# Kernel optimization log

Measured on AMD Instinct MI355X. Metric: run time of the kernel, lower is better.

## Reference

```python
import jax, jax.numpy as jnp
import numpy as np

B, H, S, D = 4, 16, 2048, 64

def setup_inputs() -> dict:
    key = jax.random.key(0)
    kq, kk, kv, km = jax.random.split(key, 4)
    q = jax.random.normal(kq, (B, H, S, D), dtype=jnp.float32)
    k = jax.random.normal(kk, (B, H, S, D), dtype=jnp.float32)
    v = jax.random.normal(kv, (B, H, S, D), dtype=jnp.float32)
    mask = jax.random.randint(km, (B, H, S, S), 0, 2, dtype=jnp.int32)
    return {"q": q, "k": k, "v": v, "mask": mask}

def reference(q, k, v, mask):
    d_k = q.shape[-1]
    scale = 1.0 / jnp.sqrt(jnp.asarray(d_k, dtype=q.dtype))
    # scores: [B, H, Sq, Sk]
    scores = jnp.einsum('bhqd,bhkd->bhqk', q, k) * scale
    scores = jnp.where(mask == 0, jnp.asarray(-10000.0, dtype=scores.dtype), scores)
    attn = jax.nn.softmax(scores, axis=-1)
    out = jnp.einsum('bhqk,bhkd->bhqd', attn, v)
    return (out, attn)
```

## Files before the change

kernel.cpp:

```cpp
#include <hip/hip_runtime.h>
#include <hip/hip_bf16.h>

typedef short bf16x8 __attribute__((ext_vector_type(8)));
typedef float f32x4 __attribute__((ext_vector_type(4)));
typedef unsigned short u16x8 __attribute__((ext_vector_type(8)));

#define DEVI static __device__ __forceinline__

constexpr int Bb = 4, Hh = 16, Ss = 2048, Dd = 64;
constexpr int BH = Bb * Hh;
constexpr float SCALE = 0.125f;
constexpr long QKV_ELEMS = (long)BH * Ss * Dd;
constexpr long MASK_ELEMS = (long)BH * Ss * Ss;

DEVI unsigned short f2bf(float f) {
  __hip_bfloat16 h = __float2bfloat16(f);
  unsigned short u;
  __builtin_memcpy(&u, &h, 2);
  return u;
}
DEVI float bflo(unsigned int u) { unsigned int x = u << 16;        float f; __builtin_memcpy(&f, &x, 4); return f; }
DEVI float bfhi(unsigned int u) { unsigned int x = u & 0xffff0000u; float f; __builtin_memcpy(&f, &x, 4); return f; }

DEVI int pidx(int q, int k) { return (q << 12) + ((k << 1) ^ ((q & 7) << 4)); }

DEVI bf16x8 cvt8(const float* p) {
  float4 a = *reinterpret_cast<const float4*>(p);
  float4 b = *reinterpret_cast<const float4*>(p + 4);
  bf16x8 r;
  r[0] = (short)f2bf(a.x); r[1] = (short)f2bf(a.y); r[2] = (short)f2bf(a.z); r[3] = (short)f2bf(a.w);
  r[4] = (short)f2bf(b.x); r[5] = (short)f2bf(b.y); r[6] = (short)f2bf(b.z); r[7] = (short)f2bf(b.w);
  return r;
}

__global__ __launch_bounds__(256) void bitpack(const int* __restrict__ mask,
                                               unsigned long long* __restrict__ bits)
{
  const long wid = (((long)blockIdx.x * 256 + threadIdx.x) >> 6);
  const int lane = threadIdx.x & 63;
  const long NW = ((long)gridDim.x * 256) >> 6;
  for (long W = wid; W < (MASK_ELEMS >> 8); W += NW) {
    const int* p = mask + (W << 8) + lane;
    const unsigned long long b0 = __ballot(__builtin_nontemporal_load(p) != 0);
    const unsigned long long b1 = __ballot(__builtin_nontemporal_load(p + 64) != 0);
    const unsigned long long b2 = __ballot(__builtin_nontemporal_load(p + 128) != 0);
    const unsigned long long b3 = __ballot(__builtin_nontemporal_load(p + 192) != 0);
    if (lane == 0) {
      ulonglong4 o; o.x = b0; o.y = b1; o.z = b2; o.w = b3;
      *reinterpret_cast<ulonglong4*>(bits + (W << 2)) = o;
    }
  }
}

__global__ __launch_bounds__(256) void cvt_qk(const float* __restrict__ q, const float* __restrict__ k,
                                              unsigned short* __restrict__ qb, unsigned short* __restrict__ kb)
{
  const long i = ((long)blockIdx.x * 256 + threadIdx.x) * 4;
  if (i >= QKV_ELEMS) return;
  const float4 a = *reinterpret_cast<const float4*>(q + i);
  ushort4 oa; oa.x = f2bf(a.x); oa.y = f2bf(a.y); oa.z = f2bf(a.z); oa.w = f2bf(a.w);
  *reinterpret_cast<ushort4*>(qb + i) = oa;
  const float4 b = *reinterpret_cast<const float4*>(k + i);
  ushort4 ob; ob.x = f2bf(b.x); ob.y = f2bf(b.y); ob.z = f2bf(b.z); ob.w = f2bf(b.w);
  *reinterpret_cast<ushort4*>(kb + i) = ob;
}

__global__ __launch_bounds__(256) void cvt_vt(const float* __restrict__ v, unsigned short* __restrict__ vt)
{
  __shared__ float tile[64][65];
  const int bh = blockIdx.x >> 5;
  const int s0 = (blockIdx.x & 31) << 6;
  const int t  = threadIdx.x;
  {
    const int c = (t & 15) << 2;
    const float* src = v + ((long)bh * Ss + s0) * Dd;
    for (int rr = (t >> 4); rr < 64; rr += 16) {
      const float4 a = *reinterpret_cast<const float4*>(src + rr * Dd + c);
      tile[rr][c] = a.x; tile[rr][c + 1] = a.y; tile[rr][c + 2] = a.z; tile[rr][c + 3] = a.w;
    }
  }
  __syncthreads();
  {
    const int d  = t >> 2;
    const int sc = (t & 3) << 4;
    unsigned short* dst = vt + ((long)bh * Dd + d) * Ss + s0 + sc;
    u16x8 v0, v1;
#pragma unroll
    for (int j = 0; j < 8; ++j) v0[j] = f2bf(tile[sc + j][d]);
#pragma unroll
    for (int j = 0; j < 8; ++j) v1[j] = f2bf(tile[sc + 8 + j][d]);
    *reinterpret_cast<u16x8*>(dst)     = v0;
    *reinterpret_cast<u16x8*>(dst + 8) = v1;
  }
}

template<bool PRE>
__global__ __launch_bounds__(512, 4)
void attn_main(const float* __restrict__ qf, const float* __restrict__ kf,
               const float* __restrict__ vf, const int* __restrict__ mask,
               const unsigned short* __restrict__ qb,
               const unsigned short* __restrict__ kbp,
               const unsigned short* __restrict__ vt,
               const unsigned long long* __restrict__ bits,
               float* __restrict__ out, float* __restrict__ attn)
{
  __shared__ __align__(16) char Pb[16 * 2048 * 2];
  __shared__ __align__(16) float Opart[2][16][64];
  __shared__ float rpart[8][16];
  __shared__ float rinv[16];

  const int tid  = threadIdx.x;
  const int wave = tid >> 6;
  const int lane = tid & 63;
  const int l15  = lane & 15;
  const int lg   = lane >> 4;

  const int bh    = blockIdx.x >> 7;
  const int qbase = (blockIdx.x & 127) << 4;

  bf16x8 qfrag0, qfrag1;
  {
    const long qrow = (long)(bh * Ss + qbase + l15) * Dd + lg * 8;
    if (PRE) {
      qfrag0 = *reinterpret_cast<const bf16x8*>(qb + qrow);
      qfrag1 = *reinterpret_cast<const bf16x8*>(qb + qrow + 32);
    } else {
      qfrag0 = cvt8(qf + qrow);
      qfrag1 = cvt8(qf + qrow + 32);
    }
  }

  float psum = 0.f;
  const long mrow = (long)(bh * Ss + qbase + l15) * Ss;

  for (int it = 0; it < 16; ++it) {
    const int key0 = (wave << 8) + (it << 4);
    bf16x8 kfrag0, kfrag1;
    const long krow = (long)(bh * Ss + key0 + l15) * Dd + lg * 8;
    if (PRE) {
      kfrag0 = *reinterpret_cast<const bf16x8*>(kbp + krow);
      kfrag1 = *reinterpret_cast<const bf16x8*>(kbp + krow + 32);
    } else {
      kfrag0 = cvt8(kf + krow);
      kfrag1 = cvt8(kf + krow + 32);
    }
    const int k0 = key0 + (lg << 2);
    unsigned mm;
    if (PRE) {
      const unsigned long long e = (unsigned long long)(mrow + k0);
      const unsigned long long w = bits[e >> 6];
      mm = (unsigned)(w >> ((int)e & 63)) & 0xFu;
    } else {
      const int4 m4 = *reinterpret_cast<const int4*>(mask + mrow + k0);
      mm = (m4.x ? 1u : 0u) | (m4.y ? 2u : 0u) | (m4.z ? 4u : 0u) | (m4.w ? 8u : 0u);
    }
    f32x4 acc = {0.f, 0.f, 0.f, 0.f};
    acc = __builtin_amdgcn_mfma_f32_16x16x32_bf16(kfrag0, qfrag0, acc, 0, 0, 0);
    acc = __builtin_amdgcn_mfma_f32_16x16x32_bf16(kfrag1, qfrag1, acc, 0, 0, 0);
    const float p0 = (mm & 1u) ? __expf(acc[0] * SCALE) : 0.f;
    const float p1 = (mm & 2u) ? __expf(acc[1] * SCALE) : 0.f;
    const float p2 = (mm & 4u) ? __expf(acc[2] * SCALE) : 0.f;
    const float p3 = (mm & 8u) ? __expf(acc[3] * SCALE) : 0.f;
    psum += (p0 + p1) + (p2 + p3);
    uint2 w2;
    w2.x = (unsigned)f2bf(p0) | ((unsigned)f2bf(p1) << 16);
    w2.y = (unsigned)f2bf(p2) | ((unsigned)f2bf(p3) << 16);
    *reinterpret_cast<uint2*>(Pb + pidx(l15, k0)) = w2;
  }

  psum += __shfl_xor(psum, 16);
  psum += __shfl_xor(psum, 32);
  if (lane < 16) rpart[wave][l15] = psum;
  __syncthreads();
  if (tid < 16) {
    float t = 0.f;
#pragma unroll
    for (int w = 0; w < 8; ++w) t += rpart[w][tid];
    rinv[tid] = (t > 0.f) ? (1.f / t) : 0.f;
  }
  __syncthreads();

  {
    const int r  = tid >> 5;
    const int cs = (tid & 31) << 3;
    const float inv = rinv[r];
    float* arow = attn + (long)(bh * Ss + qbase + r) * Ss;
#pragma unroll
    for (int it = 0; it < 8; ++it) {
      const int c0 = cs + (it << 8);
      const uint4 pk = *reinterpret_cast<const uint4*>(Pb + pidx(r, c0));
      f32x4 o0, o1;
      o0[0] = bflo(pk.x) * inv; o0[1] = bfhi(pk.x) * inv;
      o0[2] = bflo(pk.y) * inv; o0[3] = bfhi(pk.y) * inv;
      o1[0] = bflo(pk.z) * inv; o1[1] = bfhi(pk.z) * inv;
      o1[2] = bflo(pk.w) * inv; o1[3] = bfhi(pk.w) * inv;
      __builtin_nontemporal_store(o0, reinterpret_cast<f32x4*>(arow + c0));
      __builtin_nontemporal_store(o1, reinterpret_cast<f32x4*>(arow + c0 + 4));
    }
  }

  {
    const int half = wave >> 2;
    const int dcol = ((wave & 3) << 4) + l15;
    f32x4 oacc = {0.f, 0.f, 0.f, 0.f};
    const unsigned short* vrow = PRE ? (vt + (long)(bh * Dd + dcol) * Ss) : nullptr;
    const float* vcolf = PRE ? nullptr : (vf + (long)bh * Ss * Dd + dcol);
    const int kbeg = half << 10;
    for (int kk = kbeg; kk < kbeg + 1024; kk += 32) {
      const int ka = kk + (lg << 3);
      const bf16x8 afrag = *reinterpret_cast<const bf16x8*>(Pb + pidx(l15, ka));
      bf16x8 bfrag;
      if (PRE) {
        bfrag = *reinterpret_cast<const bf16x8*>(vrow + ka);
      } else {
#pragma unroll
        for (int e = 0; e < 8; ++e) bfrag[e] = (short)f2bf(vcolf[(long)(ka + e) * Dd]);
      }
      oacc = __builtin_amdgcn_mfma_f32_16x16x32_bf16(afrag, bfrag, oacc, 0, 0, 0);
    }
#pragma unroll
    for (int rg = 0; rg < 4; ++rg)
      Opart[half][(lg << 2) + rg][dcol] = oacc[rg];
  }
  __syncthreads();
  if (tid < 256) {
    const int r = tid >> 4;
    const f32x4 a = *reinterpret_cast<const f32x4*>(&Opart[0][r][(tid & 15) << 2]);
    const f32x4 b = *reinterpret_cast<const f32x4*>(&Opart[1][r][(tid & 15) << 2]);
    f32x4 t = a + b;
    t *= rinv[r];
    *reinterpret_cast<f32x4*>(out + (long)(bh * Ss + qbase) * Dd + (tid << 2)) = t;
  }
}

extern "C" void kernel_launch(void* const* d_in, const int* in_sizes, int n_in,
                              void* d_out, int out_size, void* d_ws, size_t ws_size,
                              hipStream_t stream)
{
  const float* q    = (const float*)d_in[0];
  const float* k    = (const float*)d_in[1];
  const float* v    = (const float*)d_in[2];
  const int*   mask = (const int*)d_in[3];
  float* out  = (float*)d_out;
  float* attn = out + QKV_ELEMS;

  const size_t bf16_bytes = (size_t)QKV_ELEMS * 2 * 3;
  const size_t bits_bytes = (size_t)(MASK_ELEMS >> 3);
  const size_t need = bf16_bytes + bits_bytes;
  if (ws_size >= need) {
    unsigned short* qb = (unsigned short*)d_ws;
    unsigned short* kb = qb + QKV_ELEMS;
    unsigned short* vt = kb + QKV_ELEMS;
    unsigned long long* bits = (unsigned long long*)((char*)d_ws + bf16_bytes);
    hipLaunchKernelGGL(bitpack, dim3(2048), dim3(256), 0, stream, mask, bits);
    hipLaunchKernelGGL(cvt_qk, dim3((unsigned)(QKV_ELEMS / 1024)), dim3(256), 0, stream, q, k, qb, kb);
    hipLaunchKernelGGL(cvt_vt, dim3(BH * 32), dim3(256), 0, stream, v, vt);
    hipLaunchKernelGGL((attn_main<true>), dim3(BH * 128), dim3(512), 0, stream,
                       q, k, v, mask, qb, kb, vt, bits, out, attn);
  } else {
    hipLaunchKernelGGL((attn_main<false>), dim3(BH * 128), dim3(512), 0, stream,
                       q, k, v, mask, nullptr, nullptr, nullptr, nullptr, out, attn);
  }
}
```

Measured before the change: 915.2 us.

## Fuse mask read into attention kernel and drop bitpack pre-pass

Removes the separate bitpack kernel that read the full int32 mask and wrote a bit array; the main kernel now loads the int mask directly with nontemporal vector loads, prefetching the next iteration's mask chunk. This removes one full pass over the large mask and the bits round trip. It also switches the attention-probability stores from nontemporal to regular stores. The main kernel then carries more global load traffic per iteration, which the prefetch is meant to hide.

```diff
diff --git a/kernel.cpp b/kernel.cpp
--- a/kernel.cpp
+++ b/kernel.cpp
@@ -3,6 +3,7 @@
 
 typedef short bf16x8 __attribute__((ext_vector_type(8)));
 typedef float f32x4 __attribute__((ext_vector_type(4)));
+typedef int   i32x4 __attribute__((ext_vector_type(4)));
 typedef unsigned short u16x8 __attribute__((ext_vector_type(8)));
 
 #define DEVI static __device__ __forceinline__
@@ -11,7 +12,6 @@
 constexpr int BH = Bb * Hh;
 constexpr float SCALE = 0.125f;
 constexpr long QKV_ELEMS = (long)BH * Ss * Dd;
-constexpr long MASK_ELEMS = (long)BH * Ss * Ss;
 
 DEVI unsigned short f2bf(float f) {
   __hip_bfloat16 h = __float2bfloat16(f);
@@ -31,25 +31,6 @@
   r[0] = (short)f2bf(a.x); r[1] = (short)f2bf(a.y); r[2] = (short)f2bf(a.z); r[3] = (short)f2bf(a.w);
   r[4] = (short)f2bf(b.x); r[5] = (short)f2bf(b.y); r[6] = (short)f2bf(b.z); r[7] = (short)f2bf(b.w);
   return r;
-}
-
-__global__ __launch_bounds__(256) void bitpack(const int* __restrict__ mask,
-                                               unsigned long long* __restrict__ bits)
-{
-  const long wid = (((long)blockIdx.x * 256 + threadIdx.x) >> 6);
-  const int lane = threadIdx.x & 63;
-  const long NW = ((long)gridDim.x * 256) >> 6;
-  for (long W = wid; W < (MASK_ELEMS >> 8); W += NW) {
-    const int* p = mask + (W << 8) + lane;
-    const unsigned long long b0 = __ballot(__builtin_nontemporal_load(p) != 0);
-    const unsigned long long b1 = __ballot(__builtin_nontemporal_load(p + 64) != 0);
-    const unsigned long long b2 = __ballot(__builtin_nontemporal_load(p + 128) != 0);
-    const unsigned long long b3 = __ballot(__builtin_nontemporal_load(p + 192) != 0);
-    if (lane == 0) {
-      ulonglong4 o; o.x = b0; o.y = b1; o.z = b2; o.w = b3;
-      *reinterpret_cast<ulonglong4*>(bits + (W << 2)) = o;
-    }
-  }
 }
 
 __global__ __launch_bounds__(256) void cvt_qk(const float* __restrict__ q, const float* __restrict__ k,
@@ -101,7 +82,6 @@
                const unsigned short* __restrict__ qb,
                const unsigned short* __restrict__ kbp,
                const unsigned short* __restrict__ vt,
-               const unsigned long long* __restrict__ bits,
                float* __restrict__ out, float* __restrict__ attn)
 {
   __shared__ __align__(16) char Pb[16 * 2048 * 2];
@@ -132,9 +112,15 @@
 
   float psum = 0.f;
   const long mrow = (long)(bh * Ss + qbase + l15) * Ss;
-
+  const int keyw = wave << 8;
+  const int* mbase = mask + mrow + keyw + (lg << 2);
+
+  i32x4 mcur = __builtin_nontemporal_load(reinterpret_cast<const i32x4*>(mbase));
   for (int it = 0; it < 16; ++it) {
-    const int key0 = (wave << 8) + (it << 4);
+    i32x4 mnext;
+    if (it < 15)
+      mnext = __builtin_nontemporal_load(reinterpret_cast<const i32x4*>(mbase + ((it + 1) << 4)));
+    const int key0 = keyw + (it << 4);
     bf16x8 kfrag0, kfrag1;
     const long krow = (long)(bh * Ss + key0 + l15) * Dd + lg * 8;
     if (PRE) {
@@ -144,28 +130,19 @@
       kfrag0 = cvt8(kf + krow);
       kfrag1 = cvt8(kf + krow + 32);
     }
-    const int k0 = key0 + (lg << 2);
-    unsigned mm;
-    if (PRE) {
-      const unsigned long long e = (unsigned long long)(mrow + k0);
-      const unsigned long long w = bits[e >> 6];
-      mm = (unsigned)(w >> ((int)e & 63)) & 0xFu;
-    } else {
-      const int4 m4 = *reinterpret_cast<const int4*>(mask + mrow + k0);
-      mm = (m4.x ? 1u : 0u) | (m4.y ? 2u : 0u) | (m4.z ? 4u : 0u) | (m4.w ? 8u : 0u);
-    }
     f32x4 acc = {0.f, 0.f, 0.f, 0.f};
     acc = __builtin_amdgcn_mfma_f32_16x16x32_bf16(kfrag0, qfrag0, acc, 0, 0, 0);
     acc = __builtin_amdgcn_mfma_f32_16x16x32_bf16(kfrag1, qfrag1, acc, 0, 0, 0);
-    const float p0 = (mm & 1u) ? __expf(acc[0] * SCALE) : 0.f;
-    const float p1 = (mm & 2u) ? __expf(acc[1] * SCALE) : 0.f;
-    const float p2 = (mm & 4u) ? __expf(acc[2] * SCALE) : 0.f;
-    const float p3 = (mm & 8u) ? __expf(acc[3] * SCALE) : 0.f;
+    const float p0 = mcur[0] ? __expf(acc[0] * SCALE) : 0.f;
+    const float p1 = mcur[1] ? __expf(acc[1] * SCALE) : 0.f;
+    const float p2 = mcur[2] ? __expf(acc[2] * SCALE) : 0.f;
+    const float p3 = mcur[3] ? __expf(acc[3] * SCALE) : 0.f;
     psum += (p0 + p1) + (p2 + p3);
     uint2 w2;
     w2.x = (unsigned)f2bf(p0) | ((unsigned)f2bf(p1) << 16);
     w2.y = (unsigned)f2bf(p2) | ((unsigned)f2bf(p3) << 16);
-    *reinterpret_cast<uint2*>(Pb + pidx(l15, k0)) = w2;
+    *reinterpret_cast<uint2*>(Pb + pidx(l15, key0 + (lg << 2))) = w2;
+    if (it < 15) mcur = mnext;
   }
 
   psum += __shfl_xor(psum, 16);
@@ -194,8 +171,8 @@
       o0[2] = bflo(pk.y) * inv; o0[3] = bfhi(pk.y) * inv;
       o1[0] = bflo(pk.z) * inv; o1[1] = bfhi(pk.z) * inv;
       o1[2] = bflo(pk.w) * inv; o1[3] = bfhi(pk.w) * inv;
-      __builtin_nontemporal_store(o0, reinterpret_cast<f32x4*>(arow + c0));
-      __builtin_nontemporal_store(o1, reinterpret_cast<f32x4*>(arow + c0 + 4));
+      *reinterpret_cast<f32x4*>(arow + c0)     = o0;
+      *reinterpret_cast<f32x4*>(arow + c0 + 4) = o1;
     }
   }
 
@@ -245,20 +222,16 @@
   float* attn = out + QKV_ELEMS;
 
   const size_t bf16_bytes = (size_t)QKV_ELEMS * 2 * 3;
-  const size_t bits_bytes = (size_t)(MASK_ELEMS >> 3);
-  const size_t need = bf16_bytes + bits_bytes;
-  if (ws_size >= need) {
+  if (ws_size >= bf16_bytes) {
     unsigned short* qb = (unsigned short*)d_ws;
     unsigned short* kb = qb + QKV_ELEMS;
     unsigned short* vt = kb + QKV_ELEMS;
-    unsigned long long* bits = (unsigned long long*)((char*)d_ws + bf16_bytes);
-    hipLaunchKernelGGL(bitpack, dim3(2048), dim3(256), 0, stream, mask, bits);
     hipLaunchKernelGGL(cvt_qk, dim3((unsigned)(QKV_ELEMS / 1024)), dim3(256), 0, stream, q, k, qb, kb);
     hipLaunchKernelGGL(cvt_vt, dim3(BH * 32), dim3(256), 0, stream, v, vt);
     hipLaunchKernelGGL((attn_main<true>), dim3(BH * 128), dim3(512), 0, stream,
-                       q, k, v, mask, qb, kb, vt, bits, out, attn);
+                       q, k, v, mask, qb, kb, vt, out, attn);
   } else {
     hipLaunchKernelGGL((attn_main<false>), dim3(BH * 128), dim3(512), 0, stream,
-                       q, k, v, mask, nullptr, nullptr, nullptr, nullptr, out, attn);
-  }
-}
+                       q, k, v, mask, nullptr, nullptr, nullptr, out, attn);
+  }
+}
```

Result: faster. 864.0 us (-5.6%).
